# Optimization experiments

Measured on AMD Instinct MI355X. Metric: run time of the kernel, lower is better.

## Reference

```python
import jax, jax.numpy as jnp
import numpy as np

G = 144          # fine grid size per axis
N = 200000       # active fine voxels
C_IN = 96
C_UP = C_IN // 3 # 32
C_OUT = 64
EPS = 1e-5


def _build_maps():
    rng = np.random.default_rng(0)
    lin = rng.choice(G ** 3, size=N, replace=False)
    coords = np.stack(np.unravel_index(lin, (G, G, G)), axis=1).astype(np.int64)  # [N,3]
    # coarse coords = unique parents (stride-2 downsample), inverse gives parent index per fine voxel
    coarse, up_src = np.unique(coords // 2, axis=0, return_inverse=True)
    up_off = ((coords[:, 0] % 2) * 2 + coords[:, 1] % 2) * 2 + coords[:, 2] % 2  # octant -> kernel offset id
    B = G + 2

    def enc(c):
        cc = c + 1
        return (cc[:, 0] * B + cc[:, 1]) * B + cc[:, 2]

    fkeys = enc(coords)
    order = np.argsort(fkeys)
    skeys = fkeys[order]
    offs = [(dx, dy, dz) for dx in (-1, 0, 1) for dy in (-1, 0, 1) for dz in (-1, 0, 1)]
    nbr = np.full((N, 27), -1, dtype=np.int32)
    for k, off in enumerate(offs):
        nk = enc(coords + np.asarray(off))
        pos = np.minimum(np.searchsorted(skeys, nk), N - 1)
        valid = skeys[pos] == nk
        nbr[:, k] = np.where(valid, order[pos].astype(np.int32), -1)
    return coarse.shape[0], up_src.astype(np.int32), up_off.astype(np.int32), nbr


def setup_inputs() -> dict:
    key = jax.random.key(0)
    ks = jax.random.split(key, 8)
    n_coarse, up_src, up_off, nbr = _build_maps()
    s_up = 1.0 / np.sqrt(8 * C_IN)
    s1 = 1.0 / np.sqrt(27 * C_IN)
    s2 = 1.0 / np.sqrt(27 * C_OUT)
    return {
        "x1_feats": jax.random.normal(ks[0], (n_coarse, C_IN), jnp.float32),
        "x2_feats": jax.random.normal(ks[1], (N, C_UP), jnp.float32),
        "x3_feats": jax.random.normal(ks[2], (N, C_UP), jnp.float32),
        "W_up": jax.random.normal(ks[3], (8, C_IN, C_UP), jnp.float32) * s_up,
        "g_up": jnp.ones((C_UP,), jnp.float32),
        "b_up": jnp.zeros((C_UP,), jnp.float32),
        "W1": jax.random.normal(ks[4], (27, C_IN, C_OUT), jnp.float32) * s1,
        "g1": jnp.ones((C_OUT,), jnp.float32),
        "b1": jnp.zeros((C_OUT,), jnp.float32),
        "W2": jax.random.normal(ks[5], (27, C_OUT, C_OUT), jnp.float32) * s2,
        "g2": jnp.ones((C_OUT,), jnp.float32),
        "b2": jnp.zeros((C_OUT,), jnp.float32),
        "up_src_idx": jnp.asarray(up_src),
        "up_off_id": jnp.asarray(up_off),
        "nbr_idx": jnp.asarray(nbr),
    }


def _bn_relu(x, g, b):
    # training-mode BatchNorm over active sites (biased var), then ReLU
    m = x.mean(0)
    v = x.var(0)
    return jax.nn.relu((x - m) * jax.lax.rsqrt(v + EPS) * g + b)


def _subm_conv(feats, W, nbr_idx):
    # 3x3x3 submanifold sparse conv: same coord set in/out; offset 13 is the center
    out = feats @ W[13]
    for k in range(27):
        if k == 13:
            continue
        idx = nbr_idx[:, k]
        valid = (idx >= 0)[:, None]
        g = jnp.where(valid, feats[jnp.maximum(idx, 0)], 0.0)
        out = out + g @ W[k]
    return out


def reference(x1_feats, x2_feats, x3_feats, W_up, g_up, b_up, W1, g1, b1, W2, g2, b2, up_src_idx, up_off_id, nbr_idx):
    # transposed conv k=2 s=2 (non-generative): each fine site reads its unique coarse parent,
    # weight selected by the octant offset id
    src = x1_feats[up_src_idx]  # [N, C_IN]
    up = jnp.zeros((src.shape[0], W_up.shape[2]), src.dtype)
    for k in range(8):
        up = up + jnp.where((up_off_id == k)[:, None], src @ W_up[k], 0.0)
    up = _bn_relu(up, g_up, b_up)
    x = jnp.concatenate([up, x2_feats, x3_feats], axis=1)  # [N, C_IN]
    x = _bn_relu(_subm_conv(x, W1, nbr_idx), g1, b1)
    x = _bn_relu(_subm_conv(x, W2, nbr_idx), g2, b2)
    return x
```

## Files before the change

### kernel.cpp

```cpp
#include <hip/hip_runtime.h>

typedef __attribute__((ext_vector_type(8))) short short8;
typedef __attribute__((ext_vector_type(4))) float floatx4;

__device__ inline unsigned short f2bf(float f) {
  union { float f; unsigned u; } x; x.f = f;
  unsigned r = x.u + 0x7FFFu + ((x.u >> 16) & 1u);
  return (unsigned short)(r >> 16);
}
__device__ inline float bf2f(unsigned short h) {
  union { unsigned u; float f; } x; x.u = ((unsigned)h) << 16;
  return x.f;
}

#define GLL16(g, l)                                                  \
  __builtin_amdgcn_global_load_lds(                                  \
      (const __attribute__((address_space(1))) void*)(g),            \
      (__attribute__((address_space(3))) void*)(l), 16, 0, 0)

__global__ __launch_bounds__(256) void convw_kernel(const float* __restrict__ W1,
                                                    const float* __restrict__ W2,
                                                    const float* __restrict__ Wup,
                                                    unsigned short* __restrict__ W1t,
                                                    unsigned short* __restrict__ W2t,
                                                    unsigned short* __restrict__ Wupt,
                                                    unsigned short* __restrict__ zp) {
  int idx = blockIdx.x * 256 + threadIdx.x;
  const int n1 = 27 * 96 * 64;
  const int n2 = 27 * 64 * 64;
  const int n3 = 8 * 32 * 96;
  if (idx < n1) {
    int k = idx / (96 * 64);
    int r = idx % (96 * 64);
    int q = r / 64, c = r % 64;
    W1t[((size_t)k * 64 + c) * 96 + q] = f2bf(W1[idx]);
  } else if (idx < n1 + n2) {
    int j = idx - n1;
    int k = j / 4096;
    int r = j % 4096;
    int q = r / 64, c = r % 64;
    int qs = (((q >> 3) ^ (c & 7)) << 3) | (q & 7);
    W2t[((size_t)k * 64 + c) * 64 + qs] = f2bf(W2[j]);
  } else if (idx < n1 + n2 + n3) {
    int o = idx - n1 - n2;
    int k = o / 3072;
    int r = o % 3072;
    int c = r / 96, q = r % 96;
    Wupt[o] = f2bf(Wup[((size_t)k * 96 + q) * 32 + c]);
  } else if (idx < n1 + n2 + n3 + 128) {
    zp[idx - n1 - n2 - n3] = 0;
  }
}

__global__ __launch_bounds__(256) void up_mfma_kernel(const float* __restrict__ x1,
                                                      const int* __restrict__ up_src,
                                                      const int* __restrict__ up_off,
                                                      const unsigned short* __restrict__ Wupt,
                                                      float* __restrict__ up_raw,
                                                      float* __restrict__ part1,
                                                      float* __restrict__ part2,
                                                      int N) {
  constexpr int PAD = 104;
  __shared__ unsigned short Wl[8 * 32 * PAD];
  __shared__ float wsum[4][32];
  __shared__ float wsq[4][32];

  const int tid = threadIdx.x;
  const int wv = tid >> 6;
  const int lane = tid & 63;
  const int lr = lane & 15;
  const int lg = lane >> 4;

  for (int ch = tid; ch < 8 * 32 * 12; ch += 256) {
    int kc = ch / 12, j = ch % 12;
    short8 v = *(const short8*)(Wupt + (size_t)kc * 96 + j * 8);
    *(short8*)(&Wl[kc * PAD + j * 8]) = v;
  }
  __syncthreads();

  const int nTiles = (N + 63) >> 6;
  const short8 z8 = {0, 0, 0, 0, 0, 0, 0, 0};
  float cs[2] = {0.f, 0.f}, cq[2] = {0.f, 0.f};

  for (int tile = blockIdx.x; tile < nTiles; tile += gridDim.x) {
    const int base = tile * 64;
    const int r = base + wv * 16 + lr;
    int o = -100;
    const float* ptr = x1;
    if (r < N) {
      o = up_off[r];
      ptr = x1 + (size_t)up_src[r] * 96;
    }
    short8 a_all[3];
    #pragma unroll
    for (int s = 0; s < 3; ++s) {
      float4 f0 = *(const float4*)(ptr + s * 32 + lg * 8);
      float4 f1 = *(const float4*)(ptr + s * 32 + lg * 8 + 4);
      unsigned short u[8];
      u[0] = f2bf(f0.x); u[1] = f2bf(f0.y); u[2] = f2bf(f0.z); u[3] = f2bf(f0.w);
      u[4] = f2bf(f1.x); u[5] = f2bf(f1.y); u[6] = f2bf(f1.z); u[7] = f2bf(f1.w);
      a_all[s] = *(short8*)u;
    }
    if (r >= N) {
      #pragma unroll
      for (int s = 0; s < 3; ++s) a_all[s] = z8;
    }

    floatx4 acc[2];
    acc[0] = (floatx4){0.f, 0.f, 0.f, 0.f};
    acc[1] = (floatx4){0.f, 0.f, 0.f, 0.f};
    #pragma unroll
    for (int k = 0; k < 8; ++k) {
      bool sel = (o == k);
      #pragma unroll
      for (int s = 0; s < 3; ++s) {
        short8 af = sel ? a_all[s] : z8;
        #pragma unroll
        for (int ct = 0; ct < 2; ++ct) {
          short8 bf = *(const short8*)(&Wl[(k * 32 + ct * 16 + lr) * PAD + s * 32 + lg * 8]);
          acc[ct] = __builtin_amdgcn_mfma_f32_16x16x32_bf16(af, bf, acc[ct], 0, 0, 0);
        }
      }
    }
    #pragma unroll
    for (int ct = 0; ct < 2; ++ct) {
      #pragma unroll
      for (int reg = 0; reg < 4; ++reg) {
        float v = acc[ct][reg];
        int r2 = base + wv * 16 + lg * 4 + reg;
        if (r2 < N) up_raw[(size_t)r2 * 32 + ct * 16 + lr] = v;
        cs[ct] += v;
        cq[ct] += v * v;
      }
    }
  }

  #pragma unroll
  for (int ct = 0; ct < 2; ++ct) {
    float a = cs[ct], b = cq[ct];
    a += __shfl_xor(a, 16);
    a += __shfl_xor(a, 32);
    b += __shfl_xor(b, 16);
    b += __shfl_xor(b, 32);
    if (lg == 0) {
      wsum[wv][ct * 16 + lr] = a;
      wsq[wv][ct * 16 + lr] = b;
    }
  }
  __syncthreads();
  if (tid < 32) {
    float s1 = wsum[0][tid] + wsum[1][tid] + wsum[2][tid] + wsum[3][tid];
    float s2 = wsq[0][tid] + wsq[1][tid] + wsq[2][tid] + wsq[3][tid];
    part1[(size_t)blockIdx.x * 32 + tid] = s1;
    part2[(size_t)blockIdx.x * 32 + tid] = s2;
  }
}

template <int C>
__global__ __launch_bounds__(1024) void bn_finalize(const float* __restrict__ part1,
                                                    const float* __restrict__ part2,
                                                    int nP, const float* __restrict__ g,
                                                    const float* __restrict__ b,
                                                    float* __restrict__ sb, int N) {
  constexpr int R = 1024 / C;
  __shared__ float red1[1024];
  __shared__ float red2[1024];
  const int tid = threadIdx.x;
  const int c = tid % C;
  const int r = tid / C;
  float s1 = 0.f, s2 = 0.f;
  for (int p = r; p < nP; p += R) {
    s1 += part1[(size_t)p * C + c];
    s2 += part2[(size_t)p * C + c];
  }
  red1[tid] = s1;
  red2[tid] = s2;
  __syncthreads();
  #pragma unroll
  for (int step = R / 2; step > 0; step >>= 1) {
    if (r < step) {
      red1[tid] += red1[tid + step * C];
      red2[tid] += red2[tid + step * C];
    }
    __syncthreads();
  }
  if (r == 0) {
    float mean = red1[c] / (float)N;
    float var = red2[c] / (float)N - mean * mean;
    float sc = g[c] * rsqrtf(var + 1e-5f);
    sb[c] = sc;
    sb[C + c] = b[c] - mean * sc;
  }
}

__global__ __launch_bounds__(256) void concat_kernel(const float* __restrict__ up_raw,
                                                     const float* __restrict__ x2,
                                                     const float* __restrict__ x3,
                                                     const float* __restrict__ sb,
                                                     unsigned short* __restrict__ xb,
                                                     int N) {
  int total = N * 12;
  for (int idx = blockIdx.x * 256 + threadIdx.x; idx < total; idx += gridDim.x * 256) {
    int row = idx / 12, p = idx % 12;
    float v[8];
    if (p < 4) {
      const float* s = up_raw + (size_t)row * 32 + p * 8;
      int c0 = p * 8;
      #pragma unroll
      for (int j = 0; j < 8; ++j) v[j] = fmaxf(s[j] * sb[c0 + j] + sb[32 + c0 + j], 0.f);
    } else if (p < 8) {
      const float* s = x2 + (size_t)row * 32 + (p - 4) * 8;
      #pragma unroll
      for (int j = 0; j < 8; ++j) v[j] = s[j];
    } else {
      const float* s = x3 + (size_t)row * 32 + (p - 8) * 8;
      #pragma unroll
      for (int j = 0; j < 8; ++j) v[j] = s[j];
    }
    unsigned short o[8];
    #pragma unroll
    for (int j = 0; j < 8; ++j) o[j] = f2bf(v[j]);
    ((uint4*)xb)[idx] = *(uint4*)o;
  }
}

template <int CIN, bool SWZ, bool OUTBF>
__global__ __launch_bounds__(256) void conv_kernel(const unsigned short* __restrict__ feats,
                                                   const unsigned short* __restrict__ Wt,
                                                   const int* __restrict__ nbr,
                                                   const unsigned short* __restrict__ zp,
                                                   void* __restrict__ yout,
                                                   float* __restrict__ part1,
                                                   float* __restrict__ part2,
                                                   int N) {
  constexpr int KS = CIN / 32;
  constexpr int TS = 64 * CIN;
  constexpr int CPT = (TS / 8) / 256;
  __shared__ unsigned short Bl[2 * TS];
  __shared__ float wsum[4][32];
  __shared__ float wsq[4][32];

  const int tid = threadIdx.x;
  const int wv = tid >> 6;
  const int lane = tid & 63;
  const int lr = lane & 15;
  const int lg = lane >> 4;
  const int wr = wv & 1;
  const int wc = wv >> 1;

  int nwg = gridDim.x, orig = blockIdx.x;
  int qq = nwg >> 3, rr = nwg & 7, xcd = orig & 7, jj = orig >> 3;
  int bid = (xcd < rr ? xcd * (qq + 1) : rr * (qq + 1) + (xcd - rr) * qq) + jj;
  const int base = bid * 64;

  const int row0 = base + wr * 32 + lr;
  const int row1 = row0 + 16;

  floatx4 acc[2][2];
  #pragma unroll
  for (int m = 0; m < 2; ++m)
    #pragma unroll
    for (int ct = 0; ct < 2; ++ct) acc[m][ct] = (floatx4){0.f, 0.f, 0.f, 0.f};

  auto ldnbr = [&](int t, int* nb) {
    int tt = t > 26 ? 26 : t;
    nb[0] = (row0 < N) ? nbr[(size_t)row0 * 27 + tt] : -1;
    nb[1] = (row1 < N) ? nbr[(size_t)row1 * 27 + tt] : -1;
  };
  auto gather = [&](const int* nb, short8* A) {
    #pragma unroll
    for (int m = 0; m < 2; ++m) {
      const unsigned short* src = (nb[m] >= 0) ? (feats + (size_t)nb[m] * CIN) : zp;
      #pragma unroll
      for (int s = 0; s < KS; ++s) A[m * KS + s] = *(const short8*)(src + s * 32 + lg * 8);
    }
  };
  auto stageB = [&](int t, int bufi) {
    const unsigned short* src = Wt + (size_t)t * TS;
    #pragma unroll
    for (int i = 0; i < CPT; ++i) {
      int wchunk = i * 256 + wv * 64;
      GLL16(src + (size_t)(wchunk + lane) * 8, &Bl[(size_t)bufi * TS + (size_t)wchunk * 8]);
    }
  };
  auto compute = [&](const short8* A, int bufi) {
    const unsigned short* bb = &Bl[(size_t)bufi * TS];
    #pragma unroll
    for (int s = 0; s < KS; ++s) {
      short8 bfrag[2];
      #pragma unroll
      for (int ct = 0; ct < 2; ++ct) {
        int col = wc * 32 + ct * 16 + lr;
        int off;
        if (SWZ) {
          int c0 = s * 4 + lg;
          off = col * CIN + (((c0 ^ (col & 7)) << 3));
        } else {
          off = col * CIN + s * 32 + lg * 8;
        }
        bfrag[ct] = *(const short8*)(bb + off);
      }
      #pragma unroll
      for (int m = 0; m < 2; ++m)
        #pragma unroll
        for (int ct = 0; ct < 2; ++ct)
          acc[m][ct] = __builtin_amdgcn_mfma_f32_16x16x32_bf16(A[m * KS + s], bfrag[ct], acc[m][ct], 0, 0, 0);
    }
  };

  int nb0[2], nb1[2];
  short8 A0[2 * KS], A1[2 * KS];

  ldnbr(0, nb0);
  stageB(0, 0);
  gather(nb0, A0);
  ldnbr(1, nb1);
  __syncthreads();

  #pragma unroll 1
  for (int t = 0; t < 26; t += 2) {
    stageB(t + 1, 1);
    gather(nb1, A1);
    ldnbr(t + 2, nb0);
    compute(A0, 0);
    __syncthreads();
    stageB(t + 2, 0);
    gather(nb0, A0);
    ldnbr(t + 3, nb1);
    compute(A1, 1);
    __syncthreads();
  }
  compute(A0, 0);

  float cs[2], cq[2];
  cs[0] = cs[1] = cq[0] = cq[1] = 0.f;
  #pragma unroll
  for (int m = 0; m < 2; ++m) {
    #pragma unroll
    for (int ct = 0; ct < 2; ++ct) {
      #pragma unroll
      for (int reg = 0; reg < 4; ++reg) {
        float v = acc[m][ct][reg];
        int r = base + wr * 32 + m * 16 + lg * 4 + reg;
        int col = wc * 32 + ct * 16 + lr;
        if (r < N) {
          if (OUTBF)
            ((unsigned short*)yout)[(size_t)r * 64 + col] = f2bf(v);
          else
            ((float*)yout)[(size_t)r * 64 + col] = v;
        }
        cs[ct] += v;
        cq[ct] += v * v;
      }
    }
  }
  #pragma unroll
  for (int ct = 0; ct < 2; ++ct) {
    float a = cs[ct], b = cq[ct];
    a += __shfl_xor(a, 16);
    a += __shfl_xor(a, 32);
    b += __shfl_xor(b, 16);
    b += __shfl_xor(b, 32);
    if (lg == 0) {
      wsum[wv][ct * 16 + lr] = a;
      wsq[wv][ct * 16 + lr] = b;
    }
  }
  __syncthreads();
  if (tid < 64) {
    int wcol = tid >> 5, cidx = tid & 31;
    float s1 = wsum[wcol * 2 + 0][cidx] + wsum[wcol * 2 + 1][cidx];
    float s2 = wsq[wcol * 2 + 0][cidx] + wsq[wcol * 2 + 1][cidx];
    part1[(size_t)blockIdx.x * 64 + tid] = s1;
    part2[(size_t)blockIdx.x * 64 + tid] = s2;
  }
}

__global__ __launch_bounds__(256) void apply_bn_bf16_inplace(unsigned short* __restrict__ y,
                                                             const float* __restrict__ sb,
                                                             int N) {
  int total = N * 8;
  for (int idx = blockIdx.x * 256 + threadIdx.x; idx < total; idx += gridDim.x * 256) {
    int c0 = (idx & 7) * 8;
    uint4 d = ((uint4*)y)[idx];
    unsigned short* u = (unsigned short*)&d;
    #pragma unroll
    for (int j = 0; j < 8; ++j) {
      float f = bf2f(u[j]);
      f = fmaxf(f * sb[c0 + j] + sb[64 + c0 + j], 0.f);
      u[j] = f2bf(f);
    }
    ((uint4*)y)[idx] = d;
  }
}

__global__ __launch_bounds__(256) void apply_bn_inplace(float* __restrict__ y,
                                                        const float* __restrict__ sb,
                                                        int N) {
  int total = N * 16;
  for (int idx = blockIdx.x * 256 + threadIdx.x; idx < total; idx += gridDim.x * 256) {
    int c0 = (idx & 15) * 4;
    float4 d = ((float4*)y)[idx];
    d.x = fmaxf(d.x * sb[c0 + 0] + sb[64 + c0 + 0], 0.f);
    d.y = fmaxf(d.y * sb[c0 + 1] + sb[64 + c0 + 1], 0.f);
    d.z = fmaxf(d.z * sb[c0 + 2] + sb[64 + c0 + 2], 0.f);
    d.w = fmaxf(d.w * sb[c0 + 3] + sb[64 + c0 + 3], 0.f);
    ((float4*)y)[idx] = d;
  }
}

extern "C" void kernel_launch(void* const* d_in, const int* in_sizes, int n_in,
                              void* d_out, int out_size, void* d_ws, size_t ws_size,
                              hipStream_t stream) {
  const float* x1 = (const float*)d_in[0];
  const float* x2 = (const float*)d_in[1];
  const float* x3 = (const float*)d_in[2];
  const float* Wup = (const float*)d_in[3];
  const float* gup = (const float*)d_in[4];
  const float* bup = (const float*)d_in[5];
  const float* W1 = (const float*)d_in[6];
  const float* g1 = (const float*)d_in[7];
  const float* b1 = (const float*)d_in[8];
  const float* W2 = (const float*)d_in[9];
  const float* g2 = (const float*)d_in[10];
  const float* b2 = (const float*)d_in[11];
  const int* up_src = (const int*)d_in[12];
  const int* up_off = (const int*)d_in[13];
  const int* nbr = (const int*)d_in[14];

  const int N = in_sizes[12];
  const int NB = (N + 63) / 64;

  char* ws = (char*)d_ws;
  size_t off = 0;
  auto alloc = [&](size_t bytes) -> void* {
    void* p = ws + off;
    off = (off + bytes + 255) & ~(size_t)255;
    return p;
  };

  unsigned short* xb   = (unsigned short*)alloc((size_t)N * 96 * 2);
  unsigned short* y1b  = (unsigned short*)alloc((size_t)N * 64 * 2);
  float* up_raw        = (float*)alloc((size_t)N * 32 * 4);
  unsigned short* W1t  = (unsigned short*)alloc((size_t)27 * 64 * 96 * 2);
  unsigned short* W2t  = (unsigned short*)alloc((size_t)27 * 64 * 64 * 2);
  unsigned short* Wupt = (unsigned short*)alloc((size_t)8 * 32 * 96 * 2);
  unsigned short* zp   = (unsigned short*)alloc(256);
  float* upP1          = (float*)alloc((size_t)1024 * 32 * 4);
  float* upP2          = (float*)alloc((size_t)1024 * 32 * 4);
  float* c1P1          = (float*)alloc((size_t)NB * 64 * 4);
  float* c1P2          = (float*)alloc((size_t)NB * 64 * 4);
  float* c2P1          = (float*)alloc((size_t)NB * 64 * 4);
  float* c2P2          = (float*)alloc((size_t)NB * 64 * 4);
  float* sbup          = (float*)alloc(64 * 4);
  float* sb1           = (float*)alloc(128 * 4);
  float* sb2           = (float*)alloc(128 * 4);
  (void)ws_size;

  float* out = (float*)d_out;

  convw_kernel<<<1177, 256, 0, stream>>>(W1, W2, Wup, W1t, W2t, Wupt, zp);
  up_mfma_kernel<<<1024, 256, 0, stream>>>(x1, up_src, up_off, Wupt, up_raw, upP1, upP2, N);
  bn_finalize<32><<<1, 1024, 0, stream>>>(upP1, upP2, 1024, gup, bup, sbup, N);
  concat_kernel<<<2048, 256, 0, stream>>>(up_raw, x2, x3, sbup, xb, N);
  conv_kernel<96, false, true><<<NB, 256, 0, stream>>>(xb, W1t, nbr, zp, y1b, c1P1, c1P2, N);
  bn_finalize<64><<<1, 1024, 0, stream>>>(c1P1, c1P2, NB, g1, b1, sb1, N);
  apply_bn_bf16_inplace<<<2048, 256, 0, stream>>>(y1b, sb1, N);
  conv_kernel<64, true, false><<<NB, 256, 0, stream>>>(y1b, W2t, nbr, zp, out, c2P1, c2P2, N);
  bn_finalize<64><<<1, 1024, 0, stream>>>(c2P1, c2P2, NB, g2, b2, sb2, N);
  apply_bn_inplace<<<2048, 256, 0, stream>>>(out, sb2, N);
}
```

Before: 638.5 us.

## Rework sparse conv to register weights, 128-row tiles, skip empty offsets, atomic BN stats

The conv kernel no longer stages weights in LDS with double buffering and barriers. It loads B fragments straight from global or L2 into registers, doubles the tile to 128 rows per block, and skips the MFMAs for a 16-row group when no row in the wave has a neighbour at that offset. BN partial sums are now accumulated with global atomics, and the scale and shift are computed inside the consumer kernels, which removes the three bn_finalize launches and the zero-page buffer. In exchange, the gathers lose software prefetch overlap and the weights are re-read per wave. The float atomics also make the reduction order nondeterministic.

```diff
diff --git a/kernel.cpp b/kernel.cpp
--- a/kernel.cpp
+++ b/kernel.cpp
@@ -12,11 +12,6 @@
   union { unsigned u; float f; } x; x.u = ((unsigned)h) << 16;
   return x.f;
 }
-
-#define GLL16(g, l)                                                  \
-  __builtin_amdgcn_global_load_lds(                                  \
-      (const __attribute__((address_space(1))) void*)(g),            \
-      (__attribute__((address_space(3))) void*)(l), 16, 0, 0)
 
 __global__ __launch_bounds__(256) void convw_kernel(const float* __restrict__ W1,
                                                     const float* __restrict__ W2,
@@ -24,7 +19,7 @@
                                                     unsigned short* __restrict__ W1t,
                                                     unsigned short* __restrict__ W2t,
                                                     unsigned short* __restrict__ Wupt,
-                                                    unsigned short* __restrict__ zp) {
+                                                    float* __restrict__ parts) {
   int idx = blockIdx.x * 256 + threadIdx.x;
   const int n1 = 27 * 96 * 64;
   const int n2 = 27 * 64 * 64;
@@ -39,16 +34,15 @@
     int k = j / 4096;
     int r = j % 4096;
     int q = r / 64, c = r % 64;
-    int qs = (((q >> 3) ^ (c & 7)) << 3) | (q & 7);
-    W2t[((size_t)k * 64 + c) * 64 + qs] = f2bf(W2[j]);
+    W2t[((size_t)k * 64 + c) * 64 + q] = f2bf(W2[j]);
   } else if (idx < n1 + n2 + n3) {
     int o = idx - n1 - n2;
     int k = o / 3072;
     int r = o % 3072;
     int c = r / 96, q = r % 96;
     Wupt[o] = f2bf(Wup[((size_t)k * 96 + q) * 32 + c]);
-  } else if (idx < n1 + n2 + n3 + 128) {
-    zp[idx - n1 - n2 - n3] = 0;
+  } else if (idx < n1 + n2 + n3 + 320) {
+    parts[idx - n1 - n2 - n3] = 0.f;
   }
 }
 
@@ -151,54 +145,30 @@
   if (tid < 32) {
     float s1 = wsum[0][tid] + wsum[1][tid] + wsum[2][tid] + wsum[3][tid];
     float s2 = wsq[0][tid] + wsq[1][tid] + wsq[2][tid] + wsq[3][tid];
-    part1[(size_t)blockIdx.x * 32 + tid] = s1;
-    part2[(size_t)blockIdx.x * 32 + tid] = s2;
-  }
-}
-
-template <int C>
-__global__ __launch_bounds__(1024) void bn_finalize(const float* __restrict__ part1,
-                                                    const float* __restrict__ part2,
-                                                    int nP, const float* __restrict__ g,
-                                                    const float* __restrict__ b,
-                                                    float* __restrict__ sb, int N) {
-  constexpr int R = 1024 / C;
-  __shared__ float red1[1024];
-  __shared__ float red2[1024];
-  const int tid = threadIdx.x;
-  const int c = tid % C;
-  const int r = tid / C;
-  float s1 = 0.f, s2 = 0.f;
-  for (int p = r; p < nP; p += R) {
-    s1 += part1[(size_t)p * C + c];
-    s2 += part2[(size_t)p * C + c];
-  }
-  red1[tid] = s1;
-  red2[tid] = s2;
-  __syncthreads();
-  #pragma unroll
-  for (int step = R / 2; step > 0; step >>= 1) {
-    if (r < step) {
-      red1[tid] += red1[tid + step * C];
-      red2[tid] += red2[tid + step * C];
-    }
-    __syncthreads();
-  }
-  if (r == 0) {
-    float mean = red1[c] / (float)N;
-    float var = red2[c] / (float)N - mean * mean;
-    float sc = g[c] * rsqrtf(var + 1e-5f);
-    sb[c] = sc;
-    sb[C + c] = b[c] - mean * sc;
+    atomicAdd(&part1[tid], s1);
+    atomicAdd(&part2[tid], s2);
   }
 }
 
 __global__ __launch_bounds__(256) void concat_kernel(const float* __restrict__ up_raw,
                                                      const float* __restrict__ x2,
                                                      const float* __restrict__ x3,
-                                                     const float* __restrict__ sb,
+                                                     const float* __restrict__ part1,
+                                                     const float* __restrict__ part2,
+                                                     const float* __restrict__ g,
+                                                     const float* __restrict__ b,
                                                      unsigned short* __restrict__ xb,
                                                      int N) {
+  __shared__ float ssb[64];
+  if (threadIdx.x < 32) {
+    int c = threadIdx.x;
+    float mean = part1[c] / (float)N;
+    float var = part2[c] / (float)N - mean * mean;
+    float sc = g[c] * rsqrtf(var + 1e-5f);
+    ssb[c] = sc;
+    ssb[32 + c] = b[c] - mean * sc;
+  }
+  __syncthreads();
   int total = N * 12;
   for (int idx = blockIdx.x * 256 + threadIdx.x; idx < total; idx += gridDim.x * 256) {
     int row = idx / 12, p = idx % 12;
@@ -207,7 +177,7 @@
       const float* s = up_raw + (size_t)row * 32 + p * 8;
       int c0 = p * 8;
       #pragma unroll
-      for (int j = 0; j < 8; ++j) v[j] = fmaxf(s[j] * sb[c0 + j] + sb[32 + c0 + j], 0.f);
+      for (int j = 0; j < 8; ++j) v[j] = fmaxf(s[j] * ssb[c0 + j] + ssb[32 + c0 + j], 0.f);
     } else if (p < 8) {
       const float* s = x2 + (size_t)row * 32 + (p - 4) * 8;
       #pragma unroll
@@ -224,22 +194,15 @@
   }
 }
 
-template <int CIN, bool SWZ, bool OUTBF>
+template <int CIN, bool OUTBF>
 __global__ __launch_bounds__(256) void conv_kernel(const unsigned short* __restrict__ feats,
                                                    const unsigned short* __restrict__ Wt,
                                                    const int* __restrict__ nbr,
-                                                   const unsigned short* __restrict__ zp,
                                                    void* __restrict__ yout,
                                                    float* __restrict__ part1,
                                                    float* __restrict__ part2,
                                                    int N) {
   constexpr int KS = CIN / 32;
-  constexpr int TS = 64 * CIN;
-  constexpr int CPT = (TS / 8) / 256;
-  __shared__ unsigned short Bl[2 * TS];
-  __shared__ float wsum[4][32];
-  __shared__ float wsq[4][32];
-
   const int tid = threadIdx.x;
   const int wv = tid >> 6;
   const int lane = tid & 63;
@@ -247,101 +210,78 @@
   const int lg = lane >> 4;
   const int wr = wv & 1;
   const int wc = wv >> 1;
-
-  int nwg = gridDim.x, orig = blockIdx.x;
-  int qq = nwg >> 3, rr = nwg & 7, xcd = orig & 7, jj = orig >> 3;
-  int bid = (xcd < rr ? xcd * (qq + 1) : rr * (qq + 1) + (xcd - rr) * qq) + jj;
-  const int base = bid * 64;
-
-  const int row0 = base + wr * 32 + lr;
-  const int row1 = row0 + 16;
-
-  floatx4 acc[2][2];
+  const int base = blockIdx.x * 128;
+  const int rbase = base + wr * 64 + lr;
+  const short8 z8 = {0, 0, 0, 0, 0, 0, 0, 0};
+
+  floatx4 acc[4][2];
   #pragma unroll
-  for (int m = 0; m < 2; ++m)
+  for (int m = 0; m < 4; ++m)
     #pragma unroll
     for (int ct = 0; ct < 2; ++ct) acc[m][ct] = (floatx4){0.f, 0.f, 0.f, 0.f};
 
-  auto ldnbr = [&](int t, int* nb) {
-    int tt = t > 26 ? 26 : t;
-    nb[0] = (row0 < N) ? nbr[(size_t)row0 * 27 + tt] : -1;
-    nb[1] = (row1 < N) ? nbr[(size_t)row1 * 27 + tt] : -1;
-  };
-  auto gather = [&](const int* nb, short8* A) {
-    #pragma unroll
-    for (int m = 0; m < 2; ++m) {
-      const unsigned short* src = (nb[m] >= 0) ? (feats + (size_t)nb[m] * CIN) : zp;
-      #pragma unroll
-      for (int s = 0; s < KS; ++s) A[m * KS + s] = *(const short8*)(src + s * 32 + lg * 8);
-    }
-  };
-  auto stageB = [&](int t, int bufi) {
-    const unsigned short* src = Wt + (size_t)t * TS;
-    #pragma unroll
-    for (int i = 0; i < CPT; ++i) {
-      int wchunk = i * 256 + wv * 64;
-      GLL16(src + (size_t)(wchunk + lane) * 8, &Bl[(size_t)bufi * TS + (size_t)wchunk * 8]);
-    }
-  };
-  auto compute = [&](const short8* A, int bufi) {
-    const unsigned short* bb = &Bl[(size_t)bufi * TS];
-    #pragma unroll
-    for (int s = 0; s < KS; ++s) {
-      short8 bfrag[2];
-      #pragma unroll
-      for (int ct = 0; ct < 2; ++ct) {
-        int col = wc * 32 + ct * 16 + lr;
-        int off;
-        if (SWZ) {
-          int c0 = s * 4 + lg;
-          off = col * CIN + (((c0 ^ (col & 7)) << 3));
-        } else {
-          off = col * CIN + s * 32 + lg * 8;
+  int nbc[4];
+  #pragma unroll
+  for (int m = 0; m < 4; ++m) {
+    int r = rbase + m * 16;
+    nbc[m] = (r < N) ? nbr[(size_t)r * 27] : -1;
+  }
+
+  #pragma unroll 1
+  for (int t = 0; t < 27; ++t) {
+    int nbn[4];
+    int tn = (t < 26) ? t + 1 : 26;
+    #pragma unroll
+    for (int m = 0; m < 4; ++m) {
+      int r = rbase + m * 16;
+      nbn[m] = (r < N) ? nbr[(size_t)r * 27 + tn] : -1;
+    }
+    short8 A[4][KS];
+    #pragma unroll
+    for (int m = 0; m < 4; ++m) {
+      #pragma unroll
+      for (int s = 0; s < KS; ++s) A[m][s] = z8;
+      if (nbc[m] >= 0) {
+        const unsigned short* src = feats + (size_t)nbc[m] * CIN + lg * 8;
+        #pragma unroll
+        for (int s = 0; s < KS; ++s) A[m][s] = *(const short8*)(src + s * 32);
+      }
+    }
+    bool any0 = __any(nbc[0] >= 0), any1 = __any(nbc[1] >= 0);
+    bool any2 = __any(nbc[2] >= 0), any3 = __any(nbc[3] >= 0);
+    if (any0 | any1 | any2 | any3) {
+      short8 B[2][KS];
+      const unsigned short* wsrc = Wt + ((size_t)t * 64 + wc * 32 + lr) * CIN + lg * 8;
+      #pragma unroll
+      for (int ct = 0; ct < 2; ++ct)
+        #pragma unroll
+        for (int s = 0; s < KS; ++s)
+          B[ct][s] = *(const short8*)(wsrc + ct * 16 * CIN + s * 32);
+      #pragma unroll
+      for (int m = 0; m < 4; ++m) {
+        bool anym = (m == 0) ? any0 : (m == 1) ? any1 : (m == 2) ? any2 : any3;
+        if (anym) {
+          #pragma unroll
+          for (int s = 0; s < KS; ++s) {
+            acc[m][0] = __builtin_amdgcn_mfma_f32_16x16x32_bf16(A[m][s], B[0][s], acc[m][0], 0, 0, 0);
+            acc[m][1] = __builtin_amdgcn_mfma_f32_16x16x32_bf16(A[m][s], B[1][s], acc[m][1], 0, 0, 0);
+          }
         }
-        bfrag[ct] = *(const short8*)(bb + off);
       }
-      #pragma unroll
-      for (int m = 0; m < 2; ++m)
-        #pragma unroll
-        for (int ct = 0; ct < 2; ++ct)
-          acc[m][ct] = __builtin_amdgcn_mfma_f32_16x16x32_bf16(A[m * KS + s], bfrag[ct], acc[m][ct], 0, 0, 0);
-    }
-  };
-
-  int nb0[2], nb1[2];
-  short8 A0[2 * KS], A1[2 * KS];
-
-  ldnbr(0, nb0);
-  stageB(0, 0);
-  gather(nb0, A0);
-  ldnbr(1, nb1);
-  __syncthreads();
-
-  #pragma unroll 1
-  for (int t = 0; t < 26; t += 2) {
-    stageB(t + 1, 1);
-    gather(nb1, A1);
-    ldnbr(t + 2, nb0);
-    compute(A0, 0);
-    __syncthreads();
-    stageB(t + 2, 0);
-    gather(nb0, A0);
-    ldnbr(t + 3, nb1);
-    compute(A1, 1);
-    __syncthreads();
-  }
-  compute(A0, 0);
-
-  float cs[2], cq[2];
-  cs[0] = cs[1] = cq[0] = cq[1] = 0.f;
+    }
+    #pragma unroll
+    for (int m = 0; m < 4; ++m) nbc[m] = nbn[m];
+  }
+
+  float cs[2] = {0.f, 0.f}, cq[2] = {0.f, 0.f};
   #pragma unroll
-  for (int m = 0; m < 2; ++m) {
+  for (int m = 0; m < 4; ++m) {
     #pragma unroll
     for (int ct = 0; ct < 2; ++ct) {
       #pragma unroll
       for (int reg = 0; reg < 4; ++reg) {
         float v = acc[m][ct][reg];
-        int r = base + wr * 32 + m * 16 + lg * 4 + reg;
+        int r = base + wr * 64 + m * 16 + lg * 4 + reg;
         int col = wc * 32 + ct * 16 + lr;
         if (r < N) {
           if (OUTBF)
@@ -361,24 +301,29 @@
     a += __shfl_xor(a, 32);
     b += __shfl_xor(b, 16);
     b += __shfl_xor(b, 32);
-    if (lg == 0) {
-      wsum[wv][ct * 16 + lr] = a;
-      wsq[wv][ct * 16 + lr] = b;
-    }
+    if (lane < 16) {
+      atomicAdd(&part1[wc * 32 + ct * 16 + lr], a);
+      atomicAdd(&part2[wc * 32 + ct * 16 + lr], b);
+    }
+  }
+}
+
+__global__ __launch_bounds__(256) void apply_bn_bf16_inplace(unsigned short* __restrict__ y,
+                                                             const float* __restrict__ part1,
+                                                             const float* __restrict__ part2,
+                                                             const float* __restrict__ g,
+                                                             const float* __restrict__ b,
+                                                             int N) {
+  __shared__ float ssb[128];
+  if (threadIdx.x < 64) {
+    int c = threadIdx.x;
+    float mean = part1[c] / (float)N;
+    float var = part2[c] / (float)N - mean * mean;
+    float sc = g[c] * rsqrtf(var + 1e-5f);
+    ssb[c] = sc;
+    ssb[64 + c] = b[c] - mean * sc;
   }
   __syncthreads();
-  if (tid < 64) {
-    int wcol = tid >> 5, cidx = tid & 31;
-    float s1 = wsum[wcol * 2 + 0][cidx] + wsum[wcol * 2 + 1][cidx];
-    float s2 = wsq[wcol * 2 + 0][cidx] + wsq[wcol * 2 + 1][cidx];
-    part1[(size_t)blockIdx.x * 64 + tid] = s1;
-    part2[(size_t)blockIdx.x * 64 + tid] = s2;
-  }
-}
-
-__global__ __launch_bounds__(256) void apply_bn_bf16_inplace(unsigned short* __restrict__ y,
-                                                             const float* __restrict__ sb,
-                                                             int N) {
   int total = N * 8;
   for (int idx = blockIdx.x * 256 + threadIdx.x; idx < total; idx += gridDim.x * 256) {
     int c0 = (idx & 7) * 8;
@@ -387,7 +332,7 @@
     #pragma unroll
     for (int j = 0; j < 8; ++j) {
       float f = bf2f(u[j]);
-      f = fmaxf(f * sb[c0 + j] + sb[64 + c0 + j], 0.f);
+      f = fmaxf(f * ssb[c0 + j] + ssb[64 + c0 + j], 0.f);
       u[j] = f2bf(f);
     }
     ((uint4*)y)[idx] = d;
@@ -395,16 +340,29 @@
 }
 
 __global__ __launch_bounds__(256) void apply_bn_inplace(float* __restrict__ y,
-                                                        const float* __restrict__ sb,
+                                                        const float* __restrict__ part1,
+                                                        const float* __restrict__ part2,
+                                                        const float* __restrict__ g,
+                                                        const float* __restrict__ b,
                                                         int N) {
+  __shared__ float ssb[128];
+  if (threadIdx.x < 64) {
+    int c = threadIdx.x;
+    float mean = part1[c] / (float)N;
+    float var = part2[c] / (float)N - mean * mean;
+    float sc = g[c] * rsqrtf(var + 1e-5f);
+    ssb[c] = sc;
+    ssb[64 + c] = b[c] - mean * sc;
+  }
+  __syncthreads();
   int total = N * 16;
   for (int idx = blockIdx.x * 256 + threadIdx.x; idx < total; idx += gridDim.x * 256) {
     int c0 = (idx & 15) * 4;
     float4 d = ((float4*)y)[idx];
-    d.x = fmaxf(d.x * sb[c0 + 0] + sb[64 + c0 + 0], 0.f);
-    d.y = fmaxf(d.y * sb[c0 + 1] + sb[64 + c0 + 1], 0.f);
-    d.z = fmaxf(d.z * sb[c0 + 2] + sb[64 + c0 + 2], 0.f);
-    d.w = fmaxf(d.w * sb[c0 + 3] + sb[64 + c0 + 3], 0.f);
+    d.x = fmaxf(d.x * ssb[c0 + 0] + ssb[64 + c0 + 0], 0.f);
+    d.y = fmaxf(d.y * ssb[c0 + 1] + ssb[64 + c0 + 1], 0.f);
+    d.z = fmaxf(d.z * ssb[c0 + 2] + ssb[64 + c0 + 2], 0.f);
+    d.w = fmaxf(d.w * ssb[c0 + 3] + ssb[64 + c0 + 3], 0.f);
     ((float4*)y)[idx] = d;
   }
 }
@@ -429,7 +387,7 @@
   const int* nbr = (const int*)d_in[14];
 
   const int N = in_sizes[12];
-  const int NB = (N + 63) / 64;
+  const int NB2 = (N + 127) / 128;
 
   char* ws = (char*)d_ws;
   size_t off = 0;
@@ -445,28 +403,23 @@
   unsigned short* W1t  = (unsigned short*)alloc((size_t)27 * 64 * 96 * 2);
   unsigned short* W2t  = (unsigned short*)alloc((size_t)27 * 64 * 64 * 2);
   unsigned short* Wupt = (unsigned short*)alloc((size_t)8 * 32 * 96 * 2);
-  unsigned short* zp   = (unsigned short*)alloc(256);
-  float* upP1          = (float*)alloc((size_t)1024 * 32 * 4);
-  float* upP2          = (float*)alloc((size_t)1024 * 32 * 4);
-  float* c1P1          = (float*)alloc((size_t)NB * 64 * 4);
-  float* c1P2          = (float*)alloc((size_t)NB * 64 * 4);
-  float* c2P1          = (float*)alloc((size_t)NB * 64 * 4);
-  float* c2P2          = (float*)alloc((size_t)NB * 64 * 4);
-  float* sbup          = (float*)alloc(64 * 4);
-  float* sb1           = (float*)alloc(128 * 4);
-  float* sb2           = (float*)alloc(128 * 4);
+  float* parts         = (float*)alloc(320 * 4);
   (void)ws_size;
 
+  float* upP1 = parts;
+  float* upP2 = parts + 32;
+  float* c1P1 = parts + 64;
+  float* c1P2 = parts + 128;
+  float* c2P1 = parts + 192;
+  float* c2P2 = parts + 256;
+
   float* out = (float*)d_out;
 
-  convw_kernel<<<1177, 256, 0, stream>>>(W1, W2, Wup, W1t, W2t, Wupt, zp);
+  convw_kernel<<<1178, 256, 0, stream>>>(W1, W2, Wup, W1t, W2t, Wupt, parts);
   up_mfma_kernel<<<1024, 256, 0, stream>>>(x1, up_src, up_off, Wupt, up_raw, upP1, upP2, N);
-  bn_finalize<32><<<1, 1024, 0, stream>>>(upP1, upP2, 1024, gup, bup, sbup, N);
-  concat_kernel<<<2048, 256, 0, stream>>>(up_raw, x2, x3, sbup, xb, N);
-  conv_kernel<96, false, true><<<NB, 256, 0, stream>>>(xb, W1t, nbr, zp, y1b, c1P1, c1P2, N);
-  bn_finalize<64><<<1, 1024, 0, stream>>>(c1P1, c1P2, NB, g1, b1, sb1, N);
-  apply_bn_bf16_inplace<<<2048, 256, 0, stream>>>(y1b, sb1, N);
-  conv_kernel<64, true, false><<<NB, 256, 0, stream>>>(y1b, W2t, nbr, zp, out, c2P1, c2P2, N);
-  bn_finalize<64><<<1, 1024, 0, stream>>>(c2P1, c2P2, NB, g2, b2, sb2, N);
-  apply_bn_inplace<<<2048, 256, 0, stream>>>(out, sb2, N);
-}
+  concat_kernel<<<2048, 256, 0, stream>>>(up_raw, x2, x3, upP1, upP2, gup, bup, xb, N);
+  conv_kernel<96, true><<<NB2, 256, 0, stream>>>(xb, W1t, nbr, y1b, c1P1, c1P2, N);
+  apply_bn_bf16_inplace<<<2048, 256, 0, stream>>>(y1b, c1P1, c1P2, g1, b1, N);
+  conv_kernel<64, false><<<NB2, 256, 0, stream>>>(y1b, W2t, nbr, out, c2P1, c2P2, N);
+  apply_bn_inplace<<<2048, 256, 0, stream>>>(out, c2P1, c2P2, g2, b2, N);
+}
```

Result: faster. 598.3 us (-6.3%).
